# Performance work log

Measured on AMD Instinct MI355X. Metric: run time of the kernel, lower is better.

Reference implementation:

```python
import jax, jax.numpy as jnp
import numpy as np

IN_F = 1024
OUT_F = 4096
SEARCH_SPACE = [1, 2, 4, 8, 16]  # block sizes; powers of 2 dividing both dims, capped at 16


def circ_avg(W, bs):
    """Project W [out,in] onto block-circulant structure with block size bs.

    Equivalent to trans_to_cir_meng: within each (bs x bs) block, average each
    wrap-around diagonal and rebuild a circulant block C[k, j] = c[(k - j) % bs].
    """
    q, p = W.shape[0] // bs, W.shape[1] // bs
    t = W.reshape(q, bs, p, bs).transpose(0, 2, 1, 3)  # [q, p, bs, bs]
    i = jnp.arange(bs)
    # rot[..., i, j] = t[..., i, (i + j) % bs]  (rotate rows so diagonals align in columns)
    rot = t[:, :, i[:, None], (i[:, None] + i[None, :]) % bs]  # [q, p, bs, bs]
    c = rot.mean(axis=2)  # [q, p, bs]  mean over each diagonal
    # circulant block: w[..., k, j] = c[..., (k - j) % bs]
    w = c[:, :, (i[:, None] - i[None, :]) % bs]  # [q, p, bs, bs]
    return w.transpose(0, 2, 1, 3).reshape(W.shape)


def setup_inputs() -> dict:
    key = jax.random.key(0)
    k1, k2, k3, k4 = jax.random.split(key, 4)
    x = jax.random.normal(k1, (16, 512, IN_F), dtype=jnp.float32)
    weight = jax.random.normal(k2, (OUT_F, IN_F), dtype=jnp.float32) * 0.02
    alphas = jax.random.normal(k3, (len(SEARCH_SPACE),), dtype=jnp.float32)
    bias = jax.random.normal(k4, (OUT_F,), dtype=jnp.float32) * 0.02
    return {"x": x, "weight": weight, "alphas": alphas, "bias": bias}


def reference(x, weight, alphas, bias):
    # soft NAS mixture over block sizes (tau=1, soft mode)
    a = jax.nn.softmax(alphas)
    W = a[0] * weight  # block_size 1 == original weight
    for idx, bs in enumerate(SEARCH_SPACE[1:], start=1):
        W = W + a[idx] * circ_avg(weight, bs)
    # F.linear: y = x @ W^T + b
    return jnp.einsum("bsi,oi->bso", x, W) + bias
```

## Files before the change

kernel.cpp:

```cpp
#include <hip/hip_runtime.h>

typedef __bf16 bf16;
typedef __bf16 bf16x8 __attribute__((ext_vector_type(8)));
typedef float floatx4 __attribute__((ext_vector_type(4)));

#define IN_F  1024
#define OUT_F 4096
#define M_DIM 8192
#define K_DIM 1024
#define N_DIM 4096

__device__ __forceinline__ unsigned short f2bf(float f) {
    unsigned int u = __float_as_uint(f);
    u += 0x7FFFu + ((u >> 16) & 1u);
    return (unsigned short)(u >> 16);
}

__global__ __launch_bounds__(256) void build_w_kernel(
    const float* __restrict__ W, const float* __restrict__ alphas,
    unsigned short* __restrict__ Wb)
{
    __shared__ float Wl[16 * 256];

    const int t = threadIdx.x;
    const int rb = blockIdx.x >> 2;
    const int cb = blockIdx.x & 3;
    const int row0 = rb * 16, col0 = cb * 256;

    const float4* src = (const float4*)(W + (size_t)row0 * IN_F + col0);
    #pragma unroll
    for (int j = 0; j < 4; ++j) {
        const int idx = j * 256 + t;
        const int r = idx >> 6, c4 = idx & 63;
        ((float4*)Wl)[r * 64 + c4] = src[(size_t)r * 256 + c4];
    }

    float av[5];
    float mx = -1e30f;
    #pragma unroll
    for (int j = 0; j < 5; ++j) { av[j] = alphas[j]; mx = fmaxf(mx, av[j]); }
    float s = 0.f;
    #pragma unroll
    for (int j = 0; j < 5; ++j) { av[j] = __expf(av[j] - mx); s += av[j]; }
    const float inv = 1.f / s;
    #pragma unroll
    for (int j = 0; j < 5; ++j) av[j] *= inv;

    __syncthreads();

    const int k  = t >> 4;
    const int jj = t & 15;
    unsigned short ov[16];

    #pragma unroll
    for (int jb = 0; jb < 16; ++jb) {
        const int j = jb * 16 + jj;
        float acc = av[0] * Wl[k * 256 + j];
        #pragma unroll
        for (int e = 1; e <= 4; ++e) {
            const int bs   = 1 << e;
            const int mask = bs - 1;
            const int ol = k & ~mask;
            const int il = j & ~mask;
            const int d  = (k - j) & mask;
            float ssum = 0.f;
            #pragma unroll
            for (int r = 0; r < bs; ++r)
                ssum += Wl[(ol + r) * 256 + il + ((r + d) & mask)];
            acc += av[e] * (1.0f / (float)bs) * ssum;
        }
        ov[jb] = f2bf(acc);
    }

    __syncthreads();
    unsigned short* Wls = (unsigned short*)Wl;
    #pragma unroll
    for (int jb = 0; jb < 16; ++jb)
        Wls[k * 256 + jb * 16 + jj] = ov[jb];
    __syncthreads();

    const int kr = t >> 4, cg = t & 15;
    const uint4* p = (const uint4*)(Wls + kr * 256 + cg * 16);
    uint4* dst = (uint4*)(Wb + (size_t)(row0 + kr) * IN_F + col0 + cg * 16);
    dst[0] = p[0];
    dst[1] = p[1];
}

__global__ __launch_bounds__(256) void cvt_x_kernel(
    const float* __restrict__ x, uint4* __restrict__ xb)
{
    const int t = blockIdx.x * 256 + threadIdx.x;
    const float4* xv = (const float4*)x;
    const float4 v0 = xv[2 * t];
    const float4 v1 = xv[2 * t + 1];
    uint4 o;
    o.x = (unsigned)f2bf(v0.x) | ((unsigned)f2bf(v0.y) << 16);
    o.y = (unsigned)f2bf(v0.z) | ((unsigned)f2bf(v0.w) << 16);
    o.z = (unsigned)f2bf(v1.x) | ((unsigned)f2bf(v1.y) << 16);
    o.w = (unsigned)f2bf(v1.z) | ((unsigned)f2bf(v1.w) << 16);
    xb[t] = o;
}

__global__ __launch_bounds__(256) void gemm_bt_kernel(
    const bf16* __restrict__ A, const bf16* __restrict__ B,
    const float* __restrict__ bias, float* __restrict__ C)
{
    constexpr int N = N_DIM, K = K_DIM;
    constexpr int TM = 128, TN = 128, TK = 64;

    __shared__ __align__(16) bf16 As[TM * TK];
    __shared__ __align__(16) bf16 Bs[TN * TK];

    const int t    = threadIdx.x;
    const int w    = t >> 6;
    const int l    = t & 63;
    const int quad = l >> 4;
    const int l16  = l & 15;
    const int x7   = l16 & 7;

    const int nb = N / TN;
    const int bm = blockIdx.x / nb;
    const int bn = blockIdx.x % nb;

    const int wm = (w >> 1) * 64;
    const int wn = (w & 1) * 64;

    floatx4 acc[4][4] = {};

    int crow[4], ccol[4], loff[4];
    #pragma unroll
    for (int q = 0; q < 4; ++q) {
        const int chunk = q * 256 + t;
        crow[q] = chunk >> 3;
        ccol[q] = (((chunk & 7) ^ ((chunk >> 3) & 7)) * 8);
        loff[q] = (q * 256 + (t & ~63)) * 8;
    }

    const bf16* Abase = A + (size_t)bm * TM * K;
    const bf16* Bbase = B + (size_t)bn * TN * K;

    for (int kt = 0; kt < K; kt += TK) {
        #pragma unroll
        for (int q = 0; q < 4; ++q) {
            __builtin_amdgcn_global_load_lds(
                (const __attribute__((address_space(1))) void*)(Abase + (size_t)crow[q] * K + kt + ccol[q]),
                (__attribute__((address_space(3))) void*)(As + loff[q]), 16, 0, 0);
        }
        #pragma unroll
        for (int q = 0; q < 4; ++q) {
            __builtin_amdgcn_global_load_lds(
                (const __attribute__((address_space(1))) void*)(Bbase + (size_t)crow[q] * K + kt + ccol[q]),
                (__attribute__((address_space(3))) void*)(Bs + loff[q]), 16, 0, 0);
        }
        __syncthreads();

        #pragma unroll
        for (int ks = 0; ks < 2; ++ks) {
            bf16x8 af[4], bfr[4];
            const int kx = ((ks * 4 + quad) ^ x7) * 8;
            #pragma unroll
            for (int mt = 0; mt < 4; ++mt)
                af[mt] = *(const bf16x8*)(As + (wm + mt * 16 + l16) * TK + kx);
            #pragma unroll
            for (int nt = 0; nt < 4; ++nt)
                bfr[nt] = *(const bf16x8*)(Bs + (wn + nt * 16 + l16) * TK + kx);
            #pragma unroll
            for (int mt = 0; mt < 4; ++mt)
                #pragma unroll
                for (int nt = 0; nt < 4; ++nt)
                    acc[mt][nt] = __builtin_amdgcn_mfma_f32_16x16x32_bf16(
                        af[mt], bfr[nt], acc[mt][nt], 0, 0, 0);
        }
        __syncthreads();
    }

    float bv[4];
    #pragma unroll
    for (int nt = 0; nt < 4; ++nt)
        bv[nt] = bias[bn * TN + wn + nt * 16 + l16];

    float* Cbase = C + (size_t)(bm * TM + wm) * N + bn * TN + wn;
    #pragma unroll
    for (int mt = 0; mt < 4; ++mt) {
        #pragma unroll
        for (int r = 0; r < 4; ++r) {
            float* crowp = Cbase + (size_t)(mt * 16 + quad * 4 + r) * N;
            #pragma unroll
            for (int nt = 0; nt < 4; ++nt)
                crowp[nt * 16 + l16] = acc[mt][nt][r] + bv[nt];
        }
    }
}

extern "C" void kernel_launch(void* const* d_in, const int* in_sizes, int n_in,
                              void* d_out, int out_size, void* d_ws, size_t ws_size,
                              hipStream_t stream) {
    const float* x      = (const float*)d_in[0];
    const float* weight = (const float*)d_in[1];
    const float* alphas = (const float*)d_in[2];
    const float* bias   = (const float*)d_in[3];
    float* out = (float*)d_out;

    unsigned short* Wb = (unsigned short*)d_ws;
    unsigned short* Xb = (unsigned short*)((char*)d_ws + (size_t)OUT_F * IN_F * 2);

    build_w_kernel<<<(OUT_F / 16) * (IN_F / 256), 256, 0, stream>>>(weight, alphas, Wb);
    cvt_x_kernel<<<(M_DIM * K_DIM / 8) / 256, 256, 0, stream>>>(x, (uint4*)Xb);

    const int grid = (M_DIM / 128) * (N_DIM / 128);
    gemm_bt_kernel<<<grid, 256, 0, stream>>>((const bf16*)Xb, (const bf16*)Wb, bias, out);
}
```

Before: 249.7 us.

## Precompute diagonal sums per block size and remap GEMM tiles across XCDs

The weight-build kernel now computes each block size's wrap-around diagonal sums once into shared-memory tables (D2/D4/D8/D16). Each output element then reads five table values instead of redoing up to 30 shared loads. The 1/bs scale is folded into the softmax weights. Separately, the GEMM remaps block IDs so consecutive tiles land on the same XCD (blockIdx mod 8 striding), improving L2 locality for A/B tiles; this adds shared memory use in the build kernel.

```diff
diff --git a/kernel.cpp b/kernel.cpp
--- a/kernel.cpp
+++ b/kernel.cpp
@@ -20,7 +20,11 @@
     const float* __restrict__ W, const float* __restrict__ alphas,
     unsigned short* __restrict__ Wb)
 {
-    __shared__ float Wl[16 * 256];
+    __shared__ __align__(16) float Wl[16 * 256];
+    __shared__ __align__(16) float D2[2048];
+    __shared__ float D4[1024];
+    __shared__ float D8[512];
+    __shared__ float D16[256];
 
     const int t = threadIdx.x;
     const int rb = blockIdx.x >> 2;
@@ -45,43 +49,71 @@
     const float inv = 1.f / s;
     #pragma unroll
     for (int j = 0; j < 5; ++j) av[j] *= inv;
-
-    __syncthreads();
-
-    const int k  = t >> 4;
-    const int jj = t & 15;
-    unsigned short ov[16];
-
+    #pragma unroll
+    for (int e = 1; e <= 4; ++e) av[e] *= 1.0f / (float)(1 << e);
+
+    __syncthreads();
+
+    {
+        const int c16 = t >> 4, d = t & 15;
+        float acc = 0.f;
+        #pragma unroll
+        for (int r = 0; r < 16; ++r)
+            acc += Wl[r * 256 + c16 * 16 + ((r + d) & 15)];
+        D16[t] = acc;
+    }
+    #pragma unroll
+    for (int it = 0; it < 2; ++it) {
+        const int s8 = t + it * 256;
+        const int d = s8 & 7, c8 = (s8 >> 3) & 31, r8 = s8 >> 8;
+        float acc = 0.f;
+        #pragma unroll
+        for (int r = 0; r < 8; ++r)
+            acc += Wl[(r8 * 8 + r) * 256 + c8 * 8 + ((r + d) & 7)];
+        D8[s8] = acc;
+    }
+    #pragma unroll
+    for (int it = 0; it < 4; ++it) {
+        const int s4 = t + it * 256;
+        const int d = s4 & 3, c4 = (s4 >> 2) & 63, r4 = s4 >> 8;
+        float acc = 0.f;
+        #pragma unroll
+        for (int r = 0; r < 4; ++r)
+            acc += Wl[(r4 * 4 + r) * 256 + c4 * 4 + ((r + d) & 3)];
+        D4[s4] = acc;
+    }
+    #pragma unroll
+    for (int it = 0; it < 8; ++it) {
+        const int s2 = t + it * 256;
+        const int d = s2 & 1, c2 = (s2 >> 1) & 127, r2 = s2 >> 8;
+        D2[s2] = Wl[(r2 * 2) * 256 + c2 * 2 + d]
+               + Wl[(r2 * 2 + 1) * 256 + c2 * 2 + ((1 + d) & 1)];
+    }
+
+    __syncthreads();
+
+    const int k = t >> 4, jj = t & 15;
+    float res[16];
     #pragma unroll
     for (int jb = 0; jb < 16; ++jb) {
-        const int j = jb * 16 + jj;
-        float acc = av[0] * Wl[k * 256 + j];
-        #pragma unroll
-        for (int e = 1; e <= 4; ++e) {
-            const int bs   = 1 << e;
-            const int mask = bs - 1;
-            const int ol = k & ~mask;
-            const int il = j & ~mask;
-            const int d  = (k - j) & mask;
-            float ssum = 0.f;
-            #pragma unroll
-            for (int r = 0; r < bs; ++r)
-                ssum += Wl[(ol + r) * 256 + il + ((r + d) & mask)];
-            acc += av[e] * (1.0f / (float)bs) * ssum;
-        }
-        ov[jb] = f2bf(acc);
-    }
-
-    __syncthreads();
-    unsigned short* Wls = (unsigned short*)Wl;
+        const int col = jb * 16 + jj;
+        const int dd = k - col;
+        res[jb] = av[0] * Wl[k * 256 + col]
+                + av[1] * D2[((k >> 1) * 128 + (col >> 1)) * 2 + (dd & 1)]
+                + av[2] * D4[((k >> 2) * 64  + (col >> 2)) * 4 + (dd & 3)]
+                + av[3] * D8[((k >> 3) * 32  + (col >> 3)) * 8 + (dd & 7)]
+                + av[4] * D16[(col >> 4) * 16 + (dd & 15)];
+    }
+
+    __syncthreads();
+    unsigned short* st = (unsigned short*)D2;
     #pragma unroll
     for (int jb = 0; jb < 16; ++jb)
-        Wls[k * 256 + jb * 16 + jj] = ov[jb];
-    __syncthreads();
-
-    const int kr = t >> 4, cg = t & 15;
-    const uint4* p = (const uint4*)(Wls + kr * 256 + cg * 16);
-    uint4* dst = (uint4*)(Wb + (size_t)(row0 + kr) * IN_F + col0 + cg * 16);
+        st[k * 256 + jb * 16 + jj] = f2bf(res[jb]);
+    __syncthreads();
+
+    const uint4* p = (const uint4*)(st + k * 256 + jj * 16);
+    uint4* dst = (uint4*)(Wb + (size_t)(row0 + k) * IN_F + col0 + jj * 16);
     dst[0] = p[0];
     dst[1] = p[1];
 }
@@ -107,6 +139,7 @@
 {
     constexpr int N = N_DIM, K = K_DIM;
     constexpr int TM = 128, TN = 128, TK = 64;
+    constexpr int NBLK = (M_DIM / TM) * (N_DIM / TN);
 
     __shared__ __align__(16) bf16 As[TM * TK];
     __shared__ __align__(16) bf16 Bs[TN * TK];
@@ -119,8 +152,9 @@
     const int x7   = l16 & 7;
 
     const int nb = N / TN;
-    const int bm = blockIdx.x / nb;
-    const int bn = blockIdx.x % nb;
+    const int wgid = (blockIdx.x & 7) * (NBLK >> 3) + (blockIdx.x >> 3);
+    const int bm = wgid / nb;
+    const int bn = wgid % nb;
 
     const int wm = (w >> 1) * 64;
     const int wn = (w & 1) * 64;
```

After: 248.4 us. No clear change (-0.5%).
